# Kernel tuning notes

Hardware: AMD Instinct MI355X
Metric: run time of the kernel (lower is better)

The kernel has to match this reference:

```python
import jax, jax.numpy as jnp
import numpy as np

B, L, D, H, T = 1024, 50, 4, 512, 30


def _lstm_cell(x, h, c, W_ih, W_hh, b_ih, b_hh):
    # PyTorch LSTM gate order: i, f, g, o
    g = x @ W_ih.T + b_ih + h @ W_hh.T + b_hh
    i, f, gg, o = jnp.split(g, 4, axis=-1)
    c = jax.nn.sigmoid(f) * c + jax.nn.sigmoid(i) * jnp.tanh(gg)
    h = jax.nn.sigmoid(o) * jnp.tanh(c)
    return h, c


def setup_inputs() -> dict:
    key = jax.random.key(0)
    ks = jax.random.split(key, 16)
    s = 0.05
    return {
        "input_tensor": jax.random.normal(ks[0], (B, L, D), jnp.float32),
        "target_len": T,
        "enc_W_ih": jax.random.normal(ks[1], (4 * H, D), jnp.float32) * s,
        "enc_W_hh": jax.random.normal(ks[2], (4 * H, H), jnp.float32) * s,
        "enc_b_ih": jax.random.normal(ks[3], (4 * H,), jnp.float32) * s,
        "enc_b_hh": jax.random.normal(ks[4], (4 * H,), jnp.float32) * s,
        "attn_W": jax.random.normal(ks[5], (L, H + D), jnp.float32) * s,
        "attn_b": jax.random.normal(ks[6], (L,), jnp.float32) * s,
        "comb_W": jax.random.normal(ks[7], (H, H + D), jnp.float32) * s,
        "comb_b": jax.random.normal(ks[8], (H,), jnp.float32) * s,
        "dec_W_ih": jax.random.normal(ks[9], (4 * H, H), jnp.float32) * s,
        "dec_W_hh": jax.random.normal(ks[10], (4 * H, H), jnp.float32) * s,
        "dec_b_ih": jax.random.normal(ks[11], (4 * H,), jnp.float32) * s,
        "dec_b_hh": jax.random.normal(ks[12], (4 * H,), jnp.float32) * s,
        "out_W": jax.random.normal(ks[13], (D, H), jnp.float32) * s,
        "out_b": jax.random.normal(ks[14], (D,), jnp.float32) * s,
    }


def reference(input_tensor, target_len, enc_W_ih, enc_W_hh, enc_b_ih, enc_b_hh,
              attn_W, attn_b, comb_W, comb_b,
              dec_W_ih, dec_W_hh, dec_b_ih, dec_b_hh, out_W, out_b):
    b = input_tensor.shape[0]

    # ---- encoder LSTM over input_len steps ----
    def enc_step(carry, x_t):
        h, c = carry
        h, c = _lstm_cell(x_t, h, c, enc_W_ih, enc_W_hh, enc_b_ih, enc_b_hh)
        return (h, c), h

    h0 = jnp.zeros((b, H), input_tensor.dtype)
    (h_enc, c_enc), enc_hs = jax.lax.scan(enc_step, (h0, h0),
                                          jnp.swapaxes(input_tensor, 0, 1))
    encoder_outputs = jnp.swapaxes(enc_hs, 0, 1)  # [B, L, H]

    # ---- recursive attention decoder over target_len steps ----
    def dec_step(carry, _):
        h, c, x = carry
        # faithful to torch: h.reshape(h.shape[1], -1).transpose(1, 0)
        h_r = jnp.transpose(h.reshape(H, -1))  # [B, H] (memory reinterpret)
        attn_logits = jnp.concatenate([x, h_r], axis=1) @ attn_W.T + attn_b
        attn_weights = jax.nn.softmax(attn_logits, axis=1)        # [B, L]
        attn_applied = jnp.einsum('bl,blh->bh', attn_weights, encoder_outputs)
        comb = jnp.concatenate([x, attn_applied], axis=1) @ comb_W.T + comb_b
        comb = jax.nn.relu(comb)                                  # [B, H]
        h, c = _lstm_cell(comb, h, c, dec_W_ih, dec_W_hh, dec_b_ih, dec_b_hh)
        pred = h @ out_W.T + out_b                                # [B, D]
        return (h, c, pred), pred

    dec_in0 = input_tensor[:, -1, :]
    _, preds = jax.lax.scan(dec_step, (h_enc, c_enc, dec_in0), None,
                            length=target_len)
    return jnp.swapaxes(preds, 0, 1)  # [B, target_len, D]
```

## Files before the change

kernel.cpp:

```cpp
#include <hip/hip_runtime.h>
#include <hip/hip_bf16.h>

#define Bsz   1024
#define Lseq  50
#define Din   4
#define Hd    512
#define Tlen  30
#define NWG   256

typedef __hip_bfloat16 bf16;
typedef short s16x8 __attribute__((ext_vector_type(8)));
typedef short s16x4 __attribute__((ext_vector_type(4)));
typedef float f32x4 __attribute__((ext_vector_type(4)));
typedef int   i32x2 __attribute__((ext_vector_type(2)));

__device__ __forceinline__ float bf2f(bf16 x){ return __bfloat162float(x); }
__device__ __forceinline__ bf16  f2bf(float x){ return __float2bfloat16(x); }
__device__ __forceinline__ float bfbits2f(short u){
    union { unsigned int ui; float f; } v;
    v.ui = ((unsigned int)(unsigned short)u) << 16;
    return v.f;
}
__device__ __forceinline__ short f2bfbits(float x){
    bf16 h = f2bf(x); short s; __builtin_memcpy(&s, &h, 2); return s;
}
__device__ __forceinline__ float sigm(float x){ return 1.0f/(1.0f + __expf(-x)); }
__device__ __forceinline__ float ftanh(float x){
    const float e = __expf(2.0f*x);
    return 1.0f - 2.0f/(e + 1.0f);
}
__device__ __forceinline__ i32x2 pack4(float a, float b, float c, float d){
    i32x2 v;
    v[0] = (int)(unsigned short)f2bfbits(a) | ((int)(unsigned short)f2bfbits(b) << 16);
    v[1] = (int)(unsigned short)f2bfbits(c) | ((int)(unsigned short)f2bfbits(d) << 16);
    return v;
}
__device__ __forceinline__ int pack2(float a, float b){
    return (int)(unsigned short)f2bfbits(a) | ((int)(unsigned short)f2bfbits(b) << 16);
}
__device__ __forceinline__ s16x4 sc_load_b64(const void* p){
    i32x2 v;
    asm volatile("global_load_dwordx2 %0, %1, off sc0 sc1\n\ts_waitcnt vmcnt(0)"
                 : "=v"(v) : "v"(p) : "memory");
    s16x4 r; __builtin_memcpy(&r, &v, 8); return r;
}
__device__ __forceinline__ void sc_store_b32(void* p, int v){
    asm volatile("global_store_dword %0, %1, off sc0 sc1" :: "v"(p), "v"(v) : "memory");
}

#define OFF_ABUF0   (0u)
#define OFF_ABUF1   (2u<<20)
#define OFF_HT0     (4u<<20)
#define OFF_HT1     (5u<<20)
#define OFF_ATTNAP  (8u<<20)
#define OFF_XDEC    (9u<<20)
#define OFF_FLAG    ((9u<<20) + (16u<<10))
#define OFF_COMBWR  ((9u<<20) + (32u<<10))
#define OFF_ATTNWR  ((9u<<20) + (600u<<10))
#define OFF_FLAGS   ((9u<<20) + (704u<<10))
#define OFF_WCACHE  (10u<<20)
#define OFF_ENCOUT  (18u<<20)

#define WC_INPUT 0
#define WC_EWIH  204800
#define WC_EWHH  212992
#define WC_EBIH  1261568
#define WC_EBHH  1263616
#define WC_AW    1265664
#define WC_AB    1291464
#define WC_CW    1291520
#define WC_CB    1555712
#define WC_DWIH  1556224
#define WC_DWHH  2604800
#define WC_DBIH  3653376
#define WC_DBHH  3655424
#define WC_OW    3657472
#define WC_OB    3659520
#define WC_TOTAL 3659524

__device__ __constant__ int WOFF[15] = {
    WC_INPUT, WC_EWIH, WC_EWHH, WC_EBIH, WC_EBHH, WC_AW, WC_AB, WC_CW,
    WC_CB, WC_DWIH, WC_DWHH, WC_DBIH, WC_DBHH, WC_OW, WC_OB };
__device__ __constant__ int WNUM[15] = {
    204800, 8192, 1048576, 2048, 2048, 25800, 50, 264192,
    512, 1048576, 1048576, 2048, 2048, 2048, 4 };

struct Ptrs15 { const void* p[15]; };

__global__ void probe_kernel(const unsigned int* __restrict__ w, int* flag){
    __shared__ int cnt;
    if (threadIdx.x == 0) cnt = 0;
    __syncthreads();
    int c = 0;
    for (int i = threadIdx.x; i < 4096; i += 256){
        unsigned e = (w[i] >> 7) & 0xFFu;
        c += (e >= 0x80u) ? 1 : 0;
    }
    atomicAdd(&cnt, c);
    __syncthreads();
    if (threadIdx.x == 0) *flag = (cnt > 400) ? 1 : 0;
}

__global__ __launch_bounds__(256) void convert_kernel(
    Ptrs15 srcs, const int* __restrict__ flag, bf16* __restrict__ dst)
{
    const int f = *flag;
    for (int idx = blockIdx.x*256 + threadIdx.x; idx < WC_TOTAL;
         idx += gridDim.x*256){
        int a = 0;
#pragma unroll
        for (int j = 1; j < 15; ++j) if (idx >= WOFF[j]) a = j;
        const int local = idx - WOFF[a];
        if (local >= WNUM[a]) continue;
        bf16 v;
        if (f) v = f2bf(((const float*)srcs.p[a])[local]);
        else   v = ((const bf16*)srcs.p[a])[local];
        dst[idx] = v;
    }
}

__global__ __launch_bounds__(256) void setup_kernel(
    bf16* __restrict__ Abuf0, bf16* __restrict__ Abuf1,
    bf16* __restrict__ combWr, bf16* __restrict__ attnWr,
    const bf16* __restrict__ cWc, const bf16* __restrict__ aWc)
{
    const unsigned idx = blockIdx.x*256u + threadIdx.x;
    if (idx < (unsigned)Bsz*Hd){
        const unsigned row = idx >> 9, col = idx & (Hd-1);
        const bf16 z = f2bf(0.0f);
        Abuf0[(size_t)row*1024 + Hd + col] = z;
        Abuf1[(size_t)row*1024 + Hd + col] = z;
    }
    if (idx < (unsigned)Hd*Hd)
        combWr[idx] = cWc[(size_t)(idx >> 9)*(Hd+Din) + Din + (idx & (Hd-1))];
    if (idx < (unsigned)Lseq*Hd)
        attnWr[idx] = aWc[(size_t)(idx >> 9)*(Hd+Din) + Din + (idx & (Hd-1))];
}

struct MegaP {
    const bf16 *input, *eWih, *eWhh, *ebih, *ebhh;
    const bf16 *aW, *ab, *cW, *cb, *dWih, *dWhh, *dbih, *dbhh, *oW, *ob;
    const bf16 *combWr, *attnWr;
    bf16 *A0, *A1, *encout, *attnap, *xdec;
    bf16 *hT0, *hT1;
    int *xcnt, *gcnt, *grel, *xccmap;
    const int *flag;
    void *dout;
};

#define WSTRIDE 536

__global__ __launch_bounds__(512, 2) void mega_kernel(MegaP P)
{
    __shared__ short w1_lds[64*WSTRIDE];
    __shared__ short w2_lds[64*WSTRIDE];
    __shared__ short hr_s[4][Hd];
    __shared__ float ctx_s[2][4][8][64];
    __shared__ float aw_s[4][64];
    __shared__ int   xmap_s[NWG];
    __shared__ int   info_s[2];

    const int wg = blockIdx.x, tid = threadIdx.x;
    const int wave = tid >> 6, lane = tid & 63;
    const int quad = lane >> 4, l15 = lane & 15;
    const int lbase = lane & ~3;
    const int f32out = *P.flag;

    const int grp = wg & 7, rank = wg >> 3;

    int ep = 0, gep = 0;

    auto bar_local = [&](){
        ++ep;
        __syncthreads();
        if (tid == 0){
            int* c = P.xcnt + grp*32;
            __hip_atomic_fetch_add(c, 1, __ATOMIC_RELAXED, __HIP_MEMORY_SCOPE_SYSTEM);
            while (__hip_atomic_load(c, __ATOMIC_RELAXED, __HIP_MEMORY_SCOPE_SYSTEM) < 32*ep)
                __builtin_amdgcn_s_sleep(2);
        }
        __syncthreads();
    };
    auto bar_global = [&](int fmode){
        ++ep; ++gep;
        __syncthreads();
        if (tid == 0){
            if (fmode == 2) __threadfence();
            int* c = P.xcnt + grp*32;
            __hip_atomic_fetch_add(c, 1, __ATOMIC_RELAXED, __HIP_MEMORY_SCOPE_SYSTEM);
            if (rank == 0){
                while (__hip_atomic_load(c, __ATOMIC_RELAXED, __HIP_MEMORY_SCOPE_SYSTEM) < 32*ep)
                    __builtin_amdgcn_s_sleep(2);
                if (fmode == 1) __threadfence();
                __hip_atomic_fetch_add(P.gcnt, 1, __ATOMIC_RELAXED, __HIP_MEMORY_SCOPE_SYSTEM);
                while (__hip_atomic_load(P.gcnt, __ATOMIC_RELAXED, __HIP_MEMORY_SCOPE_SYSTEM) < 8*gep)
                    __builtin_amdgcn_s_sleep(2);
                __hip_atomic_store(P.grel + grp*32, gep, __ATOMIC_RELAXED, __HIP_MEMORY_SCOPE_SYSTEM);
            } else {
                int* r = P.grel + grp*32;
                while (__hip_atomic_load(r, __ATOMIC_RELAXED, __HIP_MEMORY_SCOPE_SYSTEM) < gep)
                    __builtin_amdgcn_s_sleep(2);
            }
        }
        __syncthreads();
    };

    auto GSYNCF = [&](){
        bar_global(2);
        asm volatile("buffer_inv sc0 sc1" ::: "memory");
        __syncthreads();
    };

    if (tid == 0){
        int xcc = 0;
        asm volatile("s_getreg_b32 %0, hwreg(HW_REG_XCC_ID)" : "=s"(xcc));
        P.xccmap[wg] = xcc & 7;
    }
    GSYNCF();
    if (tid < NWG) xmap_s[tid] = P.xccmap[tid];
    __syncthreads();
    if (tid == 0){
        int ok = 1;
        for (int g = 0; g < 8; ++g){
            const int x0 = xmap_s[g];
            for (int i = 1; i < 32; ++i) ok &= (xmap_s[i*8 + g] == x0);
        }
        info_s[0] = ok;
    }
    __syncthreads();
    const int bal = info_s[0];

    auto GSYNCL = [&](){
        if (!bal){ GSYNCF(); return; }
        bar_global(1);
        asm volatile("buffer_inv" ::: "memory");
        __syncthreads();
    };
    auto XSYNC = [&](){
        if (!bal){ GSYNCF(); return; }
        bar_local();
        asm volatile("buffer_inv" ::: "memory");
    };

    bf16* bufs[2] = { P.A0, P.A1 };

    const int bm0 = grp*128, hc0 = rank*16;
    const int wm = wave >> 1, wn = wave & 1;
    const int arow0 = bm0 + wm*32 + l15;

    int ng[2];
#pragma unroll
    for (int nf = 0; nf < 2; ++nf){
        const int n = wn*32 + nf*16 + l15;
        ng[nf] = (n & 3)*Hd + hc0 + (n >> 2);
    }

    float bias_e[2], wxv_e[2][4];
#pragma unroll
    for (int nf = 0; nf < 2; ++nf){
        bias_e[nf] = bf2f(P.ebih[ng[nf]]) + bf2f(P.ebhh[ng[nf]]);
        const s16x4 t4 = *reinterpret_cast<const s16x4*>(P.eWih + (size_t)ng[nf]*Din);
#pragma unroll
        for (int d = 0; d < 4; ++d) wxv_e[nf][d] = bfbits2f(t4[d]);
    }

    for (int i = tid; i < 64*64; i += 512){
        const int col = i >> 6, k8 = (i & 63)*8;
        const int g = (col & 3)*Hd + hc0 + (col >> 2);
        const s16x8 v = *reinterpret_cast<const s16x8*>(P.eWhh + (size_t)g*Hd + k8);
        *reinterpret_cast<s16x8*>(&w2_lds[col*WSTRIDE + k8]) = v;
    }
    __syncthreads();

    float creg[2][2][4];
#pragma unroll
    for (int a = 0; a < 2; ++a)
#pragma unroll
        for (int b = 0; b < 2; ++b)
#pragma unroll
            for (int r = 0; r < 4; ++r) creg[a][b][r] = 0.0f;

    for (int t = 0; t < Lseq; ++t){
        const bf16* Ain = bufs[t&1] + Hd;
        bf16* hout = bufs[(t+1)&1] + Hd;

        f32x4 acc[2][2];
#pragma unroll
        for (int mf=0; mf<2; ++mf)
#pragma unroll
            for (int nf=0; nf<2; ++nf) acc[mf][nf] = (f32x4)0.0f;

        s16x8 afr[2], bfr[2];
#pragma unroll
        for (int sl = 0; sl < 16; ++sl){
#pragma unroll
            for (int mf = 0; mf < 2; ++mf)
                afr[mf] = *reinterpret_cast<const s16x8*>(
                    Ain + (size_t)(arow0 + mf*16)*1024 + sl*32 + quad*8);
#pragma unroll
            for (int nf = 0; nf < 2; ++nf){
                const int nl = wn*32 + nf*16 + l15;
                bfr[nf] = *reinterpret_cast<const s16x8*>(
                    &w2_lds[nl*WSTRIDE + sl*32 + quad*8]);
            }
#pragma unroll
            for (int mf = 0; mf < 2; ++mf)
#pragma unroll
                for (int nf = 0; nf < 2; ++nf)
                    acc[mf][nf] = __builtin_amdgcn_mfma_f32_16x16x32_bf16(
                        afr[mf], bfr[nf], acc[mf][nf], 0, 0, 0);
        }

#pragma unroll
        for (int mf = 0; mf < 2; ++mf){
            const int mb = bm0 + wm*32 + mf*16 + quad*4;
            s16x4 xts[4];
#pragma unroll
            for (int r = 0; r < 4; ++r)
                xts[r] = *reinterpret_cast<const s16x4*>(
                    P.input + ((size_t)(mb+r)*Lseq + t)*Din);
#pragma unroll
            for (int nf = 0; nf < 2; ++nf){
                const int n_loc = wn*32 + nf*16 + l15;
                float hvv[4];
#pragma unroll
                for (int r = 0; r < 4; ++r){
                    float gv = acc[mf][nf][r] + bias_e[nf]
                             + bfbits2f(xts[r][0])*wxv_e[nf][0]
                             + bfbits2f(xts[r][1])*wxv_e[nf][1]
                             + bfbits2f(xts[r][2])*wxv_e[nf][2]
                             + bfbits2f(xts[r][3])*wxv_e[nf][3];
                    const float gi = __shfl(gv, lbase+0);
                    const float gf = __shfl(gv, lbase+1);
                    const float gg = __shfl(gv, lbase+2);
                    const float go = __shfl(gv, lbase+3);
                    const float cn = sigm(gf)*creg[mf][nf][r] + sigm(gi)*ftanh(gg);
                    creg[mf][nf][r] = cn;
                    hvv[r] = sigm(go)*ftanh(cn);
                }
                if ((lane & 3) == 0){
                    const int hcol = hc0 + (n_loc >> 2);
#pragma unroll
                    for (int r = 0; r < 4; ++r){
                        const bf16 hb = f2bf(hvv[r]);
                        hout[(size_t)(mb+r)*1024 + hcol] = hb;
                        P.encout[((size_t)(mb+r)*Lseq + t)*Hd + hcol] = hb;
                    }
                    if (t == Lseq-1){
                        sc_store_b32(P.hT1 + ((hcol*2+0)<<9) + (mb>>1), pack2(hvv[0], hvv[2]));
                        sc_store_b32(P.hT1 + ((hcol*2+1)<<9) + (mb>>1), pack2(hvv[1], hvv[3]));
                    }
                }
            }
        }
        if (t == Lseq-1) GSYNCL(); else XSYNC();
    }

    for (int i = tid; i < 64*64; i += 512){
        const int col = i >> 6, k8 = (i & 63)*8;
        const int g = (col & 3)*Hd + hc0 + (col >> 2);
        *reinterpret_cast<s16x8*>(&w1_lds[col*WSTRIDE + k8]) =
            *reinterpret_cast<const s16x8*>(P.dWih + (size_t)g*Hd + k8);
        *reinterpret_cast<s16x8*>(&w2_lds[col*WSTRIDE + k8]) =
            *reinterpret_cast<const s16x8*>(P.dWhh + (size_t)g*Hd + k8);
    }

    float bias_d[2];
#pragma unroll
    for (int nf = 0; nf < 2; ++nf)
        bias_d[nf] = bf2f(P.dbih[ng[nf]]) + bf2f(P.dbhh[ng[nf]]);

    const int b0 = grp*128 + rank*4;
    const int s_uni = b0 >> 9;
    const int p0 = b0 & (Hd-1);

    const int rr = wave & 3, half = wave >> 2;
    s16x8 ereg[25];
    {
        const bf16* eb = P.encout + (size_t)(b0 + rr)*Lseq*Hd + lane*8;
#pragma unroll
        for (int i = 0; i < 25; ++i)
            ereg[i] = *reinterpret_cast<const s16x8*>(eb + (size_t)(half*25 + i)*Hd);
    }

    const int ccol = hc0 + l15;
    float bias_c, wxv_c[4];
    {
        bias_c = bf2f(P.cb[ccol]);
        const s16x4 t4 = *reinterpret_cast<const s16x4*>(P.cW + (size_t)ccol*(Hd+Din));
#pragma unroll
        for (int d = 0; d < 4; ++d) wxv_c[d] = bfbits2f(t4[d]);
    }
    __syncthreads();

    for (int t = 0; t < Tlen; ++t){
        const int p = t & 1;
        const bf16* hprev = bufs[p] + Hd;

        {
            const bf16* hTr = (t & 1) ? P.hT0 : P.hT1;
            const int q = tid >> 7;
            const int i0 = (tid & 127) << 2;
            const s16x4 hv = sc_load_b64(hTr + (size_t)(((p0 + q)*2 + s_uni)<<9) + i0);
            *reinterpret_cast<s16x4*>(&hr_s[q][i0]) = hv;
        }
        __syncthreads();

        if (wave < 4){
            const int b = b0 + wave;
            float x0, x1, x2, x3;
            if (t == 0){
                const bf16* xp = P.input + ((size_t)b*Lseq + (Lseq-1))*Din;
                x0 = bf2f(xp[0]); x1 = bf2f(xp[1]); x2 = bf2f(xp[2]); x3 = bf2f(xp[3]);
            } else {
                float q0=0.f, q1=0.f, q2=0.f, q3=0.f;
                const bf16* hb = hprev + (size_t)b*1024;
                for (int k = lane; k < Hd; k += 64){
                    const float hv = bf2f(hb[k]);
                    q0 += hv*bf2f(P.oW[k]);
                    q1 += hv*bf2f(P.oW[Hd+k]);
                    q2 += hv*bf2f(P.oW[2*Hd+k]);
                    q3 += hv*bf2f(P.oW[3*Hd+k]);
                }
#pragma unroll
                for (int off = 32; off; off >>= 1){
                    q0 += __shfl_down(q0, off); q1 += __shfl_down(q1, off);
                    q2 += __shfl_down(q2, off); q3 += __shfl_down(q3, off);
                }
                x0 = __shfl(q0,0) + bf2f(P.ob[0]);
                x1 = __shfl(q1,0) + bf2f(P.ob[1]);
                x2 = __shfl(q2,0) + bf2f(P.ob[2]);
                x3 = __shfl(q3,0) + bf2f(P.ob[3]);
                if (lane == 0){
                    const size_t o = ((size_t)b*Tlen + (t-1))*Din;
                    if (f32out){
                        float* dp = (float*)P.dout + o;
                        dp[0]=x0; dp[1]=x1; dp[2]=x2; dp[3]=x3;
                    } else {
                        *reinterpret_cast<i32x2*>((bf16*)P.dout + o) = pack4(x0,x1,x2,x3);
                    }
                }
            }
            if (lane == 0)
                *reinterpret_cast<i32x2*>(P.xdec + (size_t)b*Din) = pack4(x0,x1,x2,x3);

            float logit = -3.0e38f;
            if (lane < Lseq){
                float a0 = bf2f(P.ab[lane]);
                {
                    const bf16* wx = P.aW + (size_t)lane*(Hd+Din);
                    a0 += x0*bf2f(wx[0]) + x1*bf2f(wx[1]) + x2*bf2f(wx[2]) + x3*bf2f(wx[3]);
                }
                float a1 = 0.f, a2 = 0.f, a3 = 0.f;
                const bf16* wr = P.attnWr + (size_t)lane*Hd;
                for (int j = 0; j < Hd; j += 16){
                    float t4[4] = {0.f,0.f,0.f,0.f};
#pragma unroll
                    for (int q = 0; q < 4; ++q){
                        const s16x4 hw = *reinterpret_cast<const s16x4*>(&hr_s[wave][j + q*4]);
                        const s16x4 wv = *reinterpret_cast<const s16x4*>(wr + j + q*4);
                        t4[q] = bfbits2f(hw[0])*bfbits2f(wv[0]) + bfbits2f(hw[1])*bfbits2f(wv[1])
                              + bfbits2f(hw[2])*bfbits2f(wv[2]) + bfbits2f(hw[3])*bfbits2f(wv[3]);
                    }
                    a0 += t4[0]; a1 += t4[1]; a2 += t4[2]; a3 += t4[3];
                }
                logit = (a0 + a1) + (a2 + a3);
            }
            float mx = logit;
#pragma unroll
            for (int off = 32; off; off >>= 1) mx = fmaxf(mx, __shfl_xor(mx, off));
            const float e = (lane < Lseq) ? __expf(logit - mx) : 0.0f;
            float se = e;
#pragma unroll
            for (int off = 32; off; off >>= 1) se += __shfl_xor(se, off);
            aw_s[wave][lane] = e / se;
        }
        __syncthreads();

        {
            float acc8[8] = {0.f,0.f,0.f,0.f,0.f,0.f,0.f,0.f};
#pragma unroll
            for (int i = 0; i < 25; ++i){
                const float w = aw_s[rr][half*25 + i];
#pragma unroll
                for (int q = 0; q < 8; ++q) acc8[q] += w * bfbits2f(ereg[i][q]);
            }
#pragma unroll
            for (int q = 0; q < 8; ++q) ctx_s[half][rr][q][lane] = acc8[q];
        }
        __syncthreads();

        if (wave < 4){
            const int b = b0 + wave;
            s16x8 ov;
#pragma unroll
            for (int q = 0; q < 8; ++q)
                ov[q] = f2bfbits(ctx_s[0][wave][q][lane] + ctx_s[1][wave][q][lane]);
            *reinterpret_cast<s16x8*>(P.attnap + (size_t)b*Hd + lane*8) = ov;
        }
        XSYNC();

        {
            f32x4 cacc = (f32x4)0.0f;
            const bf16* Ab = P.attnap + (size_t)(bm0 + wave*16 + l15)*Hd + quad*8;
#pragma unroll
            for (int kk = 0; kk < 16; ++kk){
                const s16x8 bfr = *reinterpret_cast<const s16x8*>(
                    P.combWr + (size_t)ccol*Hd + kk*32 + quad*8);
                const s16x8 afr2 = *reinterpret_cast<const s16x8*>(Ab + kk*32);
                cacc = __builtin_amdgcn_mfma_f32_16x16x32_bf16(afr2, bfr, cacc, 0, 0, 0);
            }
            bf16* outp = bufs[p];
#pragma unroll
            for (int r = 0; r < 4; ++r){
                const int m = bm0 + wave*16 + quad*4 + r;
                const s16x4 xt = *reinterpret_cast<const s16x4*>(P.xdec + (size_t)m*Din);
                float v = cacc[r] + bias_c
                        + bfbits2f(xt[0])*wxv_c[0] + bfbits2f(xt[1])*wxv_c[1]
                        + bfbits2f(xt[2])*wxv_c[2] + bfbits2f(xt[3])*wxv_c[3];
                v = fmaxf(v, 0.0f);
                outp[(size_t)m*1024 + ccol] = f2bf(v);
            }
        }
        XSYNC();

        {
            const bf16* Ain = bufs[p];
            bf16* hout = bufs[p^1] + Hd;
            bf16* hTw = (t & 1) ? P.hT1 : P.hT0;
            f32x4 acc[2][2];
#pragma unroll
            for (int mf=0; mf<2; ++mf)
#pragma unroll
                for (int nf=0; nf<2; ++nf) acc[mf][nf] = (f32x4)0.0f;

            s16x8 afr[2], bfr[2];
#pragma unroll
            for (int sl = 0; sl < 16; ++sl){
#pragma unroll
                for (int mf = 0; mf < 2; ++mf)
                    afr[mf] = *reinterpret_cast<const s16x8*>(
                        Ain + (size_t)(arow0 + mf*16)*1024 + sl*32 + quad*8);
#pragma unroll
                for (int nf = 0; nf < 2; ++nf){
                    const int nl = wn*32 + nf*16 + l15;
                    bfr[nf] = *reinterpret_cast<const s16x8*>(
                        &w1_lds[nl*WSTRIDE + sl*32 + quad*8]);
                }
#pragma unroll
                for (int mf = 0; mf < 2; ++mf)
#pragma unroll
                    for (int nf = 0; nf < 2; ++nf)
                        acc[mf][nf] = __builtin_amdgcn_mfma_f32_16x16x32_bf16(
                            afr[mf], bfr[nf], acc[mf][nf], 0, 0, 0);
            }
#pragma unroll
            for (int sl = 0; sl < 16; ++sl){
#pragma unroll
                for (int mf = 0; mf < 2; ++mf)
                    afr[mf] = *reinterpret_cast<const s16x8*>(
                        Ain + (size_t)(arow0 + mf*16)*1024 + Hd + sl*32 + quad*8);
#pragma unroll
                for (int nf = 0; nf < 2; ++nf){
                    const int nl = wn*32 + nf*16 + l15;
                    bfr[nf] = *reinterpret_cast<const s16x8*>(
                        &w2_lds[nl*WSTRIDE + sl*32 + quad*8]);
                }
#pragma unroll
                for (int mf = 0; mf < 2; ++mf)
#pragma unroll
                    for (int nf = 0; nf < 2; ++nf)
                        acc[mf][nf] = __builtin_amdgcn_mfma_f32_16x16x32_bf16(
                            afr[mf], bfr[nf], acc[mf][nf], 0, 0, 0);
            }

#pragma unroll
            for (int mf = 0; mf < 2; ++mf){
                const int mb = bm0 + wm*32 + mf*16 + quad*4;
#pragma unroll
                for (int nf = 0; nf < 2; ++nf){
                    const int n_loc = wn*32 + nf*16 + l15;
                    float hvv[4];
#pragma unroll
                    for (int r = 0; r < 4; ++r){
                        float gv = acc[mf][nf][r] + bias_d[nf];
                        const float gi = __shfl(gv, lbase+0);
                        const float gf = __shfl(gv, lbase+1);
                        const float gg = __shfl(gv, lbase+2);
                        const float go = __shfl(gv, lbase+3);
                        const float cn = sigm(gf)*creg[mf][nf][r] + sigm(gi)*ftanh(gg);
                        creg[mf][nf][r] = cn;
                        hvv[r] = sigm(go)*ftanh(cn);
                    }
                    if ((lane & 3) == 0){
                        const int hcol = hc0 + (n_loc >> 2);
#pragma unroll
                        for (int r = 0; r < 4; ++r)
                            hout[(size_t)(mb+r)*1024 + hcol] = f2bf(hvv[r]);
                        sc_store_b32(hTw + ((hcol*2+0)<<9) + (mb>>1), pack2(hvv[0], hvv[2]));
                        sc_store_b32(hTw + ((hcol*2+1)<<9) + (mb>>1), pack2(hvv[1], hvv[3]));
                    }
                }
            }
        }
        GSYNCL();
    }

    if (wave < 4){
        const int b = b0 + wave;
        const bf16* hb = bufs[Tlen & 1] + Hd + (size_t)b*1024;
        float q0=0.f, q1=0.f, q2=0.f, q3=0.f;
        for (int k = lane; k < Hd; k += 64){
            const float hv = bf2f(hb[k]);
            q0 += hv*bf2f(P.oW[k]);
            q1 += hv*bf2f(P.oW[Hd+k]);
            q2 += hv*bf2f(P.oW[2*Hd+k]);
            q3 += hv*bf2f(P.oW[3*Hd+k]);
        }
#pragma unroll
        for (int off = 32; off; off >>= 1){
            q0 += __shfl_down(q0, off); q1 += __shfl_down(q1, off);
            q2 += __shfl_down(q2, off); q3 += __shfl_down(q3, off);
        }
        if (lane == 0){
            const size_t o = ((size_t)b*Tlen + (Tlen-1))*Din;
            const float r0 = q0 + bf2f(P.ob[0]), r1 = q1 + bf2f(P.ob[1]);
            const float r2 = q2 + bf2f(P.ob[2]), r3 = q3 + bf2f(P.ob[3]);
            if (f32out){
                float* dp = (float*)P.dout + o;
                dp[0]=r0; dp[1]=r1; dp[2]=r2; dp[3]=r3;
            } else {
                *reinterpret_cast<i32x2*>((bf16*)P.dout + o) = pack4(r0,r1,r2,r3);
            }
        }
    }
}

extern "C" void kernel_launch(void* const* d_in, const int* in_sizes, int n_in,
                              void* d_out, int out_size, void* d_ws, size_t ws_size,
                              hipStream_t stream)
{
    char* ws = (char*)d_ws;
    bf16*  Abuf0   = (bf16*)(ws + OFF_ABUF0);
    bf16*  Abuf1   = (bf16*)(ws + OFF_ABUF1);
    bf16*  hT0     = (bf16*)(ws + OFF_HT0);
    bf16*  hT1     = (bf16*)(ws + OFF_HT1);
    bf16*  attnap  = (bf16*)(ws + OFF_ATTNAP);
    bf16*  xdec    = (bf16*)(ws + OFF_XDEC);
    int*   flag    = (int*)(ws + OFF_FLAG);
    bf16*  combWr  = (bf16*)(ws + OFF_COMBWR);
    bf16*  attnWr  = (bf16*)(ws + OFF_ATTNWR);
    int*   flags   = (int*)(ws + OFF_FLAGS);
    bf16*  wc      = (bf16*)(ws + OFF_WCACHE);
    bf16*  enc_out = (bf16*)(ws + OFF_ENCOUT);

    hipMemsetAsync(flags, 0, 4096, stream);

    probe_kernel<<<1, 256, 0, stream>>>((const unsigned int*)d_in[3], flag);

    Ptrs15 srcs;
    srcs.p[0]=d_in[0];  srcs.p[1]=d_in[2];  srcs.p[2]=d_in[3];  srcs.p[3]=d_in[4];
    srcs.p[4]=d_in[5];  srcs.p[5]=d_in[6];  srcs.p[6]=d_in[7];  srcs.p[7]=d_in[8];
    srcs.p[8]=d_in[9];  srcs.p[9]=d_in[10]; srcs.p[10]=d_in[11];srcs.p[11]=d_in[12];
    srcs.p[12]=d_in[13];srcs.p[13]=d_in[14];srcs.p[14]=d_in[15];
    convert_kernel<<<1024, 256, 0, stream>>>(srcs, flag, wc);

    setup_kernel<<<2048, 256, 0, stream>>>(Abuf0, Abuf1, combWr, attnWr,
                                           wc+WC_CW, wc+WC_AW);

    MegaP P;
    P.input = wc+WC_INPUT; P.eWih = wc+WC_EWIH; P.eWhh = wc+WC_EWHH;
    P.ebih = wc+WC_EBIH;   P.ebhh = wc+WC_EBHH;
    P.aW = wc+WC_AW;  P.ab = wc+WC_AB;  P.cW = wc+WC_CW;  P.cb = wc+WC_CB;
    P.dWih = wc+WC_DWIH; P.dWhh = wc+WC_DWHH; P.dbih = wc+WC_DBIH; P.dbhh = wc+WC_DBHH;
    P.oW = wc+WC_OW;  P.ob = wc+WC_OB;
    P.combWr = combWr; P.attnWr = attnWr;
    P.A0 = Abuf0; P.A1 = Abuf1; P.encout = enc_out; P.attnap = attnap; P.xdec = xdec;
    P.hT0 = hT0; P.hT1 = hT1;
    P.xcnt = flags; P.gcnt = flags + 256; P.grel = flags + 288;
    P.xccmap = flags + 768;
    P.flag = flag; P.dout = d_out;

    mega_kernel<<<NWG, 512, 0, stream>>>(P);
}
```

Baseline: 3.154 ms.

## Hoist decoder h@W_hh MFMA before attention barrier and transpose attention weights

The recurrent h_prev @ W_hh part of the decoder gate GEMM now runs early in each timestep, right after the attention logits and before the barrier, so waves 4-7 do useful MFMA work while waves 0-3 compute softmax. This takes it off the critical path after the combine step. The attention weight matrix is also stored transposed and interleaved, padded to 64 rows, so each lane reads coalesced 4-element chunks across the K dimension. The price is four extra accumulator registers held across barriers, and the accumulators must stay live across several phases, which raises register pressure.

```diff
diff --git a/kernel.cpp b/kernel.cpp
--- a/kernel.cpp
+++ b/kernel.cpp
@@ -121,7 +121,7 @@
 
 __global__ __launch_bounds__(256) void setup_kernel(
     bf16* __restrict__ Abuf0, bf16* __restrict__ Abuf1,
-    bf16* __restrict__ combWr, bf16* __restrict__ attnWr,
+    bf16* __restrict__ combWr, bf16* __restrict__ attnWrT,
     const bf16* __restrict__ cWc, const bf16* __restrict__ aWc)
 {
     const unsigned idx = blockIdx.x*256u + threadIdx.x;
@@ -133,14 +133,18 @@
     }
     if (idx < (unsigned)Hd*Hd)
         combWr[idx] = cWc[(size_t)(idx >> 9)*(Hd+Din) + Din + (idx & (Hd-1))];
-    if (idx < (unsigned)Lseq*Hd)
-        attnWr[idx] = aWc[(size_t)(idx >> 9)*(Hd+Din) + Din + (idx & (Hd-1))];
+    if (idx < 64u*Hd){
+        const unsigned l = idx & 63u, k = idx >> 6;
+        bf16 v = f2bf(0.0f);
+        if (l < (unsigned)Lseq) v = aWc[(size_t)l*(Hd+Din) + Din + k];
+        attnWrT[((k>>2)<<8) + (l<<2) + (k&3)] = v;
+    }
 }
 
 struct MegaP {
     const bf16 *input, *eWih, *eWhh, *ebih, *ebhh;
     const bf16 *aW, *ab, *cW, *cb, *dWih, *dWhh, *dbih, *dbhh, *oW, *ob;
-    const bf16 *combWr, *attnWr;
+    const bf16 *combWr, *attnWrT;
     bf16 *A0, *A1, *encout, *attnap, *xdec;
     bf16 *hT0, *hT1;
     int *xcnt, *gcnt, *grel, *xccmap;
@@ -396,6 +400,7 @@
     for (int t = 0; t < Tlen; ++t){
         const int p = t & 1;
         const bf16* hprev = bufs[p] + Hd;
+        f32x4 acc_d[2][2];
 
         {
             const bf16* hTr = (t & 1) ? P.hT0 : P.hT1;
@@ -444,27 +449,25 @@
             if (lane == 0)
                 *reinterpret_cast<i32x2*>(P.xdec + (size_t)b*Din) = pack4(x0,x1,x2,x3);
 
+            float h0=0.f, h1=0.f, h2=0.f, h3=0.f;
+            {
+                const bf16* wrt = P.attnWrT + lane*4;
+#pragma unroll 8
+                for (int j4 = 0; j4 < 128; ++j4){
+                    const s16x4 wv = *reinterpret_cast<const s16x4*>(wrt + j4*256);
+                    const s16x4 hw = *reinterpret_cast<const s16x4*>(&hr_s[wave][j4*4]);
+                    h0 += bfbits2f(hw[0])*bfbits2f(wv[0]);
+                    h1 += bfbits2f(hw[1])*bfbits2f(wv[1]);
+                    h2 += bfbits2f(hw[2])*bfbits2f(wv[2]);
+                    h3 += bfbits2f(hw[3])*bfbits2f(wv[3]);
+                }
+            }
             float logit = -3.0e38f;
             if (lane < Lseq){
-                float a0 = bf2f(P.ab[lane]);
-                {
-                    const bf16* wx = P.aW + (size_t)lane*(Hd+Din);
-                    a0 += x0*bf2f(wx[0]) + x1*bf2f(wx[1]) + x2*bf2f(wx[2]) + x3*bf2f(wx[3]);
-                }
-                float a1 = 0.f, a2 = 0.f, a3 = 0.f;
-                const bf16* wr = P.attnWr + (size_t)lane*Hd;
-                for (int j = 0; j < Hd; j += 16){
-                    float t4[4] = {0.f,0.f,0.f,0.f};
-#pragma unroll
-                    for (int q = 0; q < 4; ++q){
-                        const s16x4 hw = *reinterpret_cast<const s16x4*>(&hr_s[wave][j + q*4]);
-                        const s16x4 wv = *reinterpret_cast<const s16x4*>(wr + j + q*4);
-                        t4[q] = bfbits2f(hw[0])*bfbits2f(wv[0]) + bfbits2f(hw[1])*bfbits2f(wv[1])
-                              + bfbits2f(hw[2])*bfbits2f(wv[2]) + bfbits2f(hw[3])*bfbits2f(wv[3]);
-                    }
-                    a0 += t4[0]; a1 += t4[1]; a2 += t4[2]; a3 += t4[3];
-                }
-                logit = (a0 + a1) + (a2 + a3);
+                const bf16* wx = P.aW + (size_t)lane*(Hd+Din);
+                const float a0 = bf2f(P.ab[lane])
+                    + x0*bf2f(wx[0]) + x1*bf2f(wx[1]) + x2*bf2f(wx[2]) + x3*bf2f(wx[3]);
+                logit = (a0 + h0) + (h1 + h2) + h3;
             }
             float mx = logit;
 #pragma unroll
@@ -474,6 +477,33 @@
 #pragma unroll
             for (int off = 32; off; off >>= 1) se += __shfl_xor(se, off);
             aw_s[wave][lane] = e / se;
+        }
+
+        {
+#pragma unroll
+            for (int mf=0; mf<2; ++mf)
+#pragma unroll
+                for (int nf=0; nf<2; ++nf) acc_d[mf][nf] = (f32x4)0.0f;
+            s16x8 afr[2], bfr[2];
+#pragma unroll
+            for (int sl = 0; sl < 16; ++sl){
+#pragma unroll
+                for (int mf = 0; mf < 2; ++mf)
+                    afr[mf] = *reinterpret_cast<const s16x8*>(
+                        hprev + (size_t)(arow0 + mf*16)*1024 + sl*32 + quad*8);
+#pragma unroll
+                for (int nf = 0; nf < 2; ++nf){
+                    const int nl = wn*32 + nf*16 + l15;
+                    bfr[nf] = *reinterpret_cast<const s16x8*>(
+                        &w2_lds[nl*WSTRIDE + sl*32 + quad*8]);
+                }
+#pragma unroll
+                for (int mf = 0; mf < 2; ++mf)
+#pragma unroll
+                    for (int nf = 0; nf < 2; ++nf)
+                        acc_d[mf][nf] = __builtin_amdgcn_mfma_f32_16x16x32_bf16(
+                            afr[mf], bfr[nf], acc_d[mf][nf], 0, 0, 0);
+            }
         }
         __syncthreads();
 
@@ -528,11 +558,6 @@
             const bf16* Ain = bufs[p];
             bf16* hout = bufs[p^1] + Hd;
             bf16* hTw = (t & 1) ? P.hT1 : P.hT0;
-            f32x4 acc[2][2];
-#pragma unroll
-            for (int mf=0; mf<2; ++mf)
-#pragma unroll
-                for (int nf=0; nf<2; ++nf) acc[mf][nf] = (f32x4)0.0f;
 
             s16x8 afr[2], bfr[2];
 #pragma unroll
@@ -551,27 +576,8 @@
                 for (int mf = 0; mf < 2; ++mf)
 #pragma unroll
                     for (int nf = 0; nf < 2; ++nf)
-                        acc[mf][nf] = __builtin_amdgcn_mfma_f32_16x16x32_bf16(
-                            afr[mf], bfr[nf], acc[mf][nf], 0, 0, 0);
-            }
-#pragma unroll
-            for (int sl = 0; sl < 16; ++sl){
-#pragma unroll
-                for (int mf = 0; mf < 2; ++mf)
-                    afr[mf] = *reinterpret_cast<const s16x8*>(
-                        Ain + (size_t)(arow0 + mf*16)*1024 + Hd + sl*32 + quad*8);
-#pragma unroll
-                for (int nf = 0; nf < 2; ++nf){
-                    const int nl = wn*32 + nf*16 + l15;
-                    bfr[nf] = *reinterpret_cast<const s16x8*>(
-                        &w2_lds[nl*WSTRIDE + sl*32 + quad*8]);
-                }
-#pragma unroll
-                for (int mf = 0; mf < 2; ++mf)
-#pragma unroll
-                    for (int nf = 0; nf < 2; ++nf)
-                        acc[mf][nf] = __builtin_amdgcn_mfma_f32_16x16x32_bf16(
-                            afr[mf], bfr[nf], acc[mf][nf], 0, 0, 0);
+                        acc_d[mf][nf] = __builtin_amdgcn_mfma_f32_16x16x32_bf16(
+                            afr[mf], bfr[nf], acc_d[mf][nf], 0, 0, 0);
             }
 
 #pragma unroll
@@ -583,7 +589,7 @@
                     float hvv[4];
 #pragma unroll
                     for (int r = 0; r < 4; ++r){
-                        float gv = acc[mf][nf][r] + bias_d[nf];
+                        float gv = acc_d[mf][nf][r] + bias_d[nf];
                         const float gi = __shfl(gv, lbase+0);
                         const float gf = __shfl(gv, lbase+1);
                         const float gg = __shfl(gv, lbase+2);
@@ -649,7 +655,7 @@
     bf16*  xdec    = (bf16*)(ws + OFF_XDEC);
     int*   flag    = (int*)(ws + OFF_FLAG);
     bf16*  combWr  = (bf16*)(ws + OFF_COMBWR);
-    bf16*  attnWr  = (bf16*)(ws + OFF_ATTNWR);
+    bf16*  attnWrT = (bf16*)(ws + OFF_ATTNWR);
     int*   flags   = (int*)(ws + OFF_FLAGS);
     bf16*  wc      = (bf16*)(ws + OFF_WCACHE);
     bf16*  enc_out = (bf16*)(ws + OFF_ENCOUT);
@@ -665,7 +671,7 @@
     srcs.p[12]=d_in[13];srcs.p[13]=d_in[14];srcs.p[14]=d_in[15];
     convert_kernel<<<1024, 256, 0, stream>>>(srcs, flag, wc);
 
-    setup_kernel<<<2048, 256, 0, stream>>>(Abuf0, Abuf1, combWr, attnWr,
+    setup_kernel<<<2048, 256, 0, stream>>>(Abuf0, Abuf1, combWr, attnWrT,
                                            wc+WC_CW, wc+WC_AW);
 
     MegaP P;
@@ -674,7 +680,7 @@
     P.aW = wc+WC_AW;  P.ab = wc+WC_AB;  P.cW = wc+WC_CW;  P.cb = wc+WC_CB;
     P.dWih = wc+WC_DWIH; P.dWhh = wc+WC_DWHH; P.dbih = wc+WC_DBIH; P.dbhh = wc+WC_DBHH;
     P.oW = wc+WC_OW;  P.ob = wc+WC_OB;
-    P.combWr = combWr; P.attnWr = attnWr;
+    P.combWr = combWr; P.attnWrT = attnWrT;
     P.A0 = Abuf0; P.A1 = Abuf1; P.encout = enc_out; P.attnap = attnap; P.xdec = xdec;
     P.hT0 = hT0; P.hT1 = hT1;
     P.xcnt = flags; P.gcnt = flags + 256; P.grel = flags + 288;
```

Result: slower. 3.770 ms (+19.5%).
